# Optimization experiments

Measured on AMD Instinct MI355X. Metric: run time of the kernel, lower is better.

The kernel has to match this reference:

```python
import jax, jax.numpy as jnp
import numpy as np

DIM = 768
HEADS = 12
HEAD_DIM = DIM // HEADS
SCALE = HEAD_DIM ** -0.5


def setup_inputs() -> dict:
    key = jax.random.key(0)
    k_x, k_qkv, k_ow, k_ob = jax.random.split(key, 4)
    B, N = 8, 1024
    x = jax.random.normal(k_x, (B, N, DIM), dtype=jnp.float32)
    # nn.Linear weights: out = x @ W.T + b; store torch-layout [out, in]
    w_qkv = jax.random.normal(k_qkv, (3 * DIM, DIM), dtype=jnp.float32) * (DIM ** -0.5)
    w_out = jax.random.normal(k_ow, (DIM, DIM), dtype=jnp.float32) * (DIM ** -0.5)
    b_out = jax.random.normal(k_ob, (DIM,), dtype=jnp.float32) * 0.01
    return {"x": x, "w_qkv": w_qkv, "w_out": w_out, "b_out": b_out}


def reference(x, w_qkv, w_out, b_out):
    B, N, C = x.shape
    qkv = jnp.einsum('bnc,dc->bnd', x, w_qkv)            # [B, N, 3C]
    qkv = qkv.reshape(B, N, 3, HEADS, HEAD_DIM)
    qkv = jnp.transpose(qkv, (2, 0, 3, 1, 4))            # [3, B, H, N, Dh]
    q, k, v = qkv[0], qkv[1], qkv[2]
    attn = jnp.einsum('bhqd,bhkd->bhqk', q, k) * SCALE   # [B, H, N, N]
    attn = jax.nn.softmax(attn, axis=-1)
    o = jnp.einsum('bhqk,bhkd->bhqd', attn, v)           # [B, H, N, Dh]
    o = jnp.transpose(o, (0, 2, 1, 3)).reshape(B, N, C)
    return jnp.einsum('bnc,dc->bnd', o, w_out) + b_out
```

## Files before the change

### kernel.cpp

```cpp
#include <hip/hip_runtime.h>

#define B_ 8
#define N_ 1024
#define DIM_ 768
#define H_ 12
#define DH_ 64
#define M_ (B_ * N_)
#define NQKV_ (3 * DIM_)
#define SCL_ 0.18033688011112042f

typedef unsigned short u16;
typedef unsigned int u32;
typedef __attribute__((ext_vector_type(8))) unsigned short u16x8;
typedef __attribute__((ext_vector_type(4))) unsigned short u16x4;
typedef __attribute__((ext_vector_type(8))) short bf16x8;
typedef __attribute__((ext_vector_type(4))) float f32x4;

__device__ __forceinline__ u16 f2bf(float f) {
  u32 u = __builtin_bit_cast(u32, f);
  u += 0x7fffu + ((u >> 16) & 1u);
  return (u16)(u >> 16);
}
__device__ __forceinline__ float bf2f(u16 v) {
  u32 u = ((u32)v) << 16;
  return __builtin_bit_cast(float, u);
}
__device__ __forceinline__ u32 cvtpk_bf16(float lo, float hi) {
  u32 r;
  asm("v_cvt_pk_bf16_f32 %0, %1, %2" : "=v"(r) : "v"(lo), "v"(hi));
  return r;
}
__device__ __forceinline__ void async16(const void* g, void* l) {
  __builtin_amdgcn_global_load_lds(
      (const __attribute__((address_space(1))) unsigned int*)g,
      (__attribute__((address_space(3))) unsigned int*)l, 16, 0, 0);
}
#define WAIT4_BAR()                                     \
  asm volatile("s_waitcnt vmcnt(4)" ::: "memory");      \
  __builtin_amdgcn_s_barrier();                         \
  __builtin_amdgcn_sched_barrier(0)
#define WAIT0_BAR()                                     \
  asm volatile("s_waitcnt vmcnt(0)" ::: "memory");      \
  __builtin_amdgcn_s_barrier();                         \
  __builtin_amdgcn_sched_barrier(0)
#define RING_ADV(o) (o) = ((o) == 16384) ? 0 : (o) + 8192

__global__ __launch_bounds__(256) void cast_bf16_k(const float* __restrict__ in,
                                                   u16* __restrict__ out, int n4) {
  int i = blockIdx.x * 256 + threadIdx.x;
  if (i >= n4) return;
  float4 v = reinterpret_cast<const float4*>(in)[i];
  u16x4 o;
  o.x = f2bf(v.x); o.y = f2bf(v.y); o.z = f2bf(v.z); o.w = f2bf(v.w);
  reinterpret_cast<u16x4*>(out)[i] = o;
}

__device__ __forceinline__ void gemm_step(const char* lA, const char* lB,
                                          const int (&aoff)[4],
                                          const int (&boff)[4],
                                          f32x4 (&acc)[4][4]) {
  bf16x8 af[4], bfr[4];
#pragma unroll
  for (int m = 0; m < 4; ++m) af[m] = *(const bf16x8*)(lA + aoff[m]);
#pragma unroll
  for (int n = 0; n < 4; ++n) bfr[n] = *(const bf16x8*)(lB + boff[n]);
#pragma unroll
  for (int m = 0; m < 4; ++m)
#pragma unroll
    for (int n = 0; n < 4; ++n)
      acc[m][n] = __builtin_amdgcn_mfma_f32_16x16x32_bf16(af[m], bfr[n],
                                                          acc[m][n], 0, 0, 0);
}

template <bool OUT_BF16, bool BIAS, bool VSPLIT>
__global__ __launch_bounds__(256) void gemm_bt_k(
    const u16* __restrict__ A, const u16* __restrict__ Bm,
    void* __restrict__ Cv, const float* __restrict__ bias, int K, int ldc,
    u16* __restrict__ vT) {
  __shared__ u16 As[3][128 * 32];
  __shared__ u16 Bs[3][128 * 32];
  const int t = threadIdx.x;
  const int lane = t & 63;
  const int wid = t >> 6;
  const int id = blockIdx.x;
  const int xcd = id & 7, r = id >> 3;
  const int brow = ((xcd << 3) | (r & 7)) << 7;
  const int bcol = (r >> 3) << 7;
  const int wrow = (wid >> 1) << 6;
  const int wcol = (wid & 1) << 6;

  f32x4 acc[4][4];
#pragma unroll
  for (int m = 0; m < 4; ++m)
#pragma unroll
    for (int n = 0; n < 4; ++n) acc[m][n] = (f32x4){0.f, 0.f, 0.f, 0.f};

  const int loff0 = t << 4, loff1 = (t + 256) << 4;
  const int r0 = loff0 >> 6, r1 = loff1 >> 6;
  const int s0 = ((((loff0 >> 4) & 3) ^ (r0 & 3)) << 3);
  const int s1 = ((((loff1 >> 4) & 3) ^ (r1 & 3)) << 3);
  const u16* pA0 = A + (size_t)(brow + r0) * K + s0;
  const u16* pA1 = A + (size_t)(brow + r1) * K + s1;
  const u16* pB0 = Bm + (size_t)(bcol + r0) * K + s0;
  const u16* pB1 = Bm + (size_t)(bcol + r1) * K + s1;
  char* lA = (char*)As;
  char* lB = (char*)Bs;
  int sb = 0, cb = 0;

#define GSTAGE()                                  \
  do {                                            \
    async16(pA0, lA + sb + loff0);                \
    async16(pA1, lA + sb + loff1);                \
    async16(pB0, lB + sb + loff0);                \
    async16(pB1, lB + sb + loff1);                \
    pA0 += 32; pA1 += 32; pB0 += 32; pB1 += 32;   \
    RING_ADV(sb);                                 \
  } while (0)

  const int kb = (lane >> 4) << 4;
  int aoff[4], boff[4];
#pragma unroll
  for (int m = 0; m < 4; ++m) {
    int ra = wrow + (m << 4) + (lane & 15);
    aoff[m] = (ra << 6) + (kb ^ ((ra & 3) << 4));
    int rb = wcol + (m << 4) + (lane & 15);
    boff[m] = (rb << 6) + (kb ^ ((rb & 3) << 4));
  }

  const int nkt = K >> 5;
  GSTAGE();
  GSTAGE();
  for (int kt = 0; kt < nkt - 2; ++kt) {
    WAIT4_BAR();
    GSTAGE();
    gemm_step(lA + cb, lB + cb, aoff, boff, acc);
    RING_ADV(cb);
  }
  WAIT4_BAR();
  gemm_step(lA + cb, lB + cb, aoff, boff, acc);
  RING_ADV(cb);
  WAIT0_BAR();
  gemm_step(lA + cb, lB + cb, aoff, boff, acc);
#undef GSTAGE

  const int crow = brow + wrow + ((lane >> 4) << 2);
  const int ccol0 = bcol + wcol + (lane & 15);
  if (VSPLIT && bcol >= 2 * DIM_) {
#pragma unroll
    for (int n = 0; n < 4; ++n) {
      int colh = ccol0 + (n << 4) - 2 * DIM_;
      int h = colh >> 6, d = colh & 63;
#pragma unroll
      for (int m = 0; m < 4; ++m) {
        int row0 = crow + (m << 4);
        int bb = row0 >> 10, nn = row0 & 1023;
        int hbl = bb * H_ + h;
        uint2 pk;
        pk.x = (u32)f2bf(acc[m][n][0]) | ((u32)f2bf(acc[m][n][1]) << 16);
        pk.y = (u32)f2bf(acc[m][n][2]) | ((u32)f2bf(acc[m][n][3]) << 16);
        *(uint2*)(vT + (((size_t)(hbl * 64 + d)) << 10) + nn) = pk;
      }
    }
    return;
  }
#pragma unroll
  for (int m = 0; m < 4; ++m)
#pragma unroll
    for (int n = 0; n < 4; ++n) {
      int col = ccol0 + (n << 4);
      float bv = BIAS ? bias[col] : 0.f;
#pragma unroll
      for (int j = 0; j < 4; ++j) {
        int row = crow + (m << 4) + j;
        if (OUT_BF16)
          ((u16*)Cv)[(size_t)row * ldc + col] = f2bf(acc[m][n][j]);
        else
          ((float*)Cv)[(size_t)row * ldc + col] = acc[m][n][j] + bv;
      }
    }
}

__device__ __forceinline__ void attn_tile(const char* lk, const char* lv,
                                          char* lp, const bf16x8 (&qf)[2],
                                          f32x4 (&oacc)[4], float& mrow,
                                          float& lrow, const int rowB,
                                          const int xsw, const int x0,
                                          const int x1, const int g) {
  f32x4 s4[4];
#pragma unroll
  for (int n = 0; n < 4; ++n) s4[n] = (f32x4){0.f, 0.f, 0.f, 0.f};
  __builtin_amdgcn_s_setprio(1);
#pragma unroll
  for (int n = 0; n < 4; ++n) {
    bf16x8 kf0 = *(const bf16x8*)(lk + (n << 11) + rowB + x0);
    s4[n] = __builtin_amdgcn_mfma_f32_16x16x32_bf16(kf0, qf[0], s4[n], 0, 0, 0);
    bf16x8 kf1 = *(const bf16x8*)(lk + (n << 11) + rowB + x1);
    s4[n] = __builtin_amdgcn_mfma_f32_16x16x32_bf16(kf1, qf[1], s4[n], 0, 0, 0);
  }
  __builtin_amdgcn_s_setprio(0);

  float mx;
  {
    float a0 = fmaxf(fmaxf(s4[0][0], s4[0][1]), fmaxf(s4[0][2], s4[0][3]));
    float a1 = fmaxf(fmaxf(s4[1][0], s4[1][1]), fmaxf(s4[1][2], s4[1][3]));
    float a2 = fmaxf(fmaxf(s4[2][0], s4[2][1]), fmaxf(s4[2][2], s4[2][3]));
    float a3 = fmaxf(fmaxf(s4[3][0], s4[3][1]), fmaxf(s4[3][2], s4[3][3]));
    mx = fmaxf(fmaxf(a0, a1), fmaxf(a2, a3));
    mx = fmaxf(mx, __shfl_xor(mx, 16, 64));
    mx = fmaxf(mx, __shfl_xor(mx, 32, 64));
  }
  if (!__all(mx - mrow <= 8.f)) {
    float mn = fmaxf(mrow, mx);
    float al = __builtin_amdgcn_exp2f(mrow - mn);
    mrow = mn;
    lrow *= al;
    float alj[4];
#pragma unroll
    for (int j = 0; j < 4; ++j) alj[j] = __shfl(al, (g << 2) + j, 64);
#pragma unroll
    for (int d = 0; d < 4; ++d)
#pragma unroll
      for (int j = 0; j < 4; ++j) oacc[d][j] *= alj[j];
  }

  float p[4][4];
  float ps = 0.f;
#pragma unroll
  for (int n = 0; n < 4; ++n)
#pragma unroll
    for (int j = 0; j < 4; ++j) {
      p[n][j] = __builtin_amdgcn_exp2f(s4[n][j] - mrow);
      ps += p[n][j];
    }
  ps += __shfl_xor(ps, 16, 64);
  ps += __shfl_xor(ps, 32, 64);
  lrow += ps;

#pragma unroll
  for (int n = 0; n < 4; ++n) {
    uint2 pk;
    pk.x = cvtpk_bf16(p[n][0], p[n][1]);
    pk.y = cvtpk_bf16(p[n][2], p[n][3]);
    *(uint2*)(lp + rowB + (((n << 5) + (g << 3)) ^ xsw)) = pk;
  }

  bf16x8 pf0 = *(const bf16x8*)(lp + rowB + x0);
  bf16x8 pf1 = *(const bf16x8*)(lp + rowB + x1);
  __builtin_amdgcn_s_setprio(1);
#pragma unroll
  for (int dt = 0; dt < 4; ++dt) {
    bf16x8 vf0 = *(const bf16x8*)(lv + (dt << 11) + rowB + x0);
    oacc[dt] = __builtin_amdgcn_mfma_f32_16x16x32_bf16(pf0, vf0, oacc[dt], 0, 0, 0);
    bf16x8 vf1 = *(const bf16x8*)(lv + (dt << 11) + rowB + x1);
    oacc[dt] = __builtin_amdgcn_mfma_f32_16x16x32_bf16(pf1, vf1, oacc[dt], 0, 0, 0);
  }
  __builtin_amdgcn_s_setprio(0);
}

__global__ __launch_bounds__(256) void attn_k(const u16* __restrict__ qkv,
                                              const u16* __restrict__ vT,
                                              u16* __restrict__ ob) {
  __shared__ u16 Ks[3][64 * 64];
  __shared__ u16 Vt[3][64 * 64];
  __shared__ u16 Ps[4][16 * 64];
  const int t = threadIdx.x;
  const int lane = t & 63;
  const int w = t >> 6;
  const int g = lane >> 4;
  const int q15 = lane & 15;

  const int orig = blockIdx.x;
  const int sub = orig >> 3;
  const int hb = (orig & 7) * 12 + (sub >> 4);
  const int qt = sub & 15;
  const int b = hb / H_;
  const int h = hb - b * H_;
  const int rowbase = b * N_;
  const int qcol = h * DH_;
  const int kcol = DIM_ + qcol;

  bf16x8 qf[2];
  {
    const int qrow = rowbase + (qt << 6) + (w << 4) + q15;
    const u16* src = qkv + (size_t)qrow * NQKV_ + qcol + (g << 3);
#pragma unroll
    for (int ks = 0; ks < 2; ++ks) {
      u16x8 raw = *(const u16x8*)(src + ks * 32);
      bf16x8 o;
#pragma unroll
      for (int j = 0; j < 8; ++j) o[j] = (short)f2bf(bf2f(raw[j]) * SCL_);
      qf[ks] = o;
    }
  }

  float mrow = -1e30f, lrow = 0.f;
  f32x4 oacc[4];
#pragma unroll
  for (int d = 0; d < 4; ++d) oacc[d] = (f32x4){0.f, 0.f, 0.f, 0.f};

  const int sr = t >> 3;
  const int c8 = t & 7;
  const int loff0 = t << 4, loff1 = (t + 256) << 4;
  const u16* pk0 = qkv + (size_t)(rowbase + sr) * NQKV_ + kcol + ((c8 ^ (sr & 7)) << 3);
  const u16* pk1 = qkv + (size_t)(rowbase + sr + 32) * NQKV_ + kcol + ((c8 ^ (sr & 7)) << 3);
  const u16* pv0 = vT + (((size_t)(hb * 64 + sr)) << 10) + ((c8 ^ (sr & 7)) << 3);
  const u16* pv1 = vT + (((size_t)(hb * 64 + sr + 32)) << 10) + ((c8 ^ (sr & 7)) << 3);
  char* lk0 = (char*)Ks;
  char* lv0 = (char*)Vt;
  char* lp = (char*)Ps + (w << 11);
  int sb = 0, cb = 0;

#define ASTAGE()                                           \
  do {                                                     \
    async16(pk0, lk0 + sb + loff0);                        \
    async16(pk1, lk0 + sb + loff1);                        \
    async16(pv0, lv0 + sb + loff0);                        \
    async16(pv1, lv0 + sb + loff1);                        \
    pk0 += (size_t)64 * NQKV_; pk1 += (size_t)64 * NQKV_;  \
    pv0 += 64; pv1 += 64;                                  \
    RING_ADV(sb);                                          \
  } while (0)

  const int rowB = q15 << 7;
  const int xsw = (q15 & 7) << 4;
  const int x0 = (g << 4) ^ xsw;
  const int x1 = (64 + (g << 4)) ^ xsw;

  ASTAGE();
  ASTAGE();
  for (int kvt = 0; kvt < 14; ++kvt) {
    WAIT4_BAR();
    ASTAGE();
    attn_tile(lk0 + cb, lv0 + cb, lp, qf, oacc, mrow, lrow, rowB, xsw, x0, x1, g);
    RING_ADV(cb);
  }
  WAIT4_BAR();
  attn_tile(lk0 + cb, lv0 + cb, lp, qf, oacc, mrow, lrow, rowB, xsw, x0, x1, g);
  RING_ADV(cb);
  WAIT0_BAR();
  attn_tile(lk0 + cb, lv0 + cb, lp, qf, oacc, mrow, lrow, rowB, xsw, x0, x1, g);
#undef ASTAGE

  float rl = 1.f / lrow;
  float rlj[4];
#pragma unroll
  for (int j = 0; j < 4; ++j) rlj[j] = __shfl(rl, (g << 2) + j, 64);
  const int orow0 = rowbase + (qt << 6) + (w << 4) + (g << 2);
#pragma unroll
  for (int dt = 0; dt < 4; ++dt) {
    int col = qcol + (dt << 4) + q15;
#pragma unroll
    for (int j = 0; j < 4; ++j)
      ob[(size_t)(orow0 + j) * DIM_ + col] = f2bf(oacc[dt][j] * rlj[j]);
  }
}

extern "C" void kernel_launch(void* const* d_in, const int* in_sizes, int n_in,
                              void* d_out, int out_size, void* d_ws, size_t ws_size,
                              hipStream_t stream) {
  const float* x = (const float*)d_in[0];
  const float* w_qkv = (const float*)d_in[1];
  const float* w_out = (const float*)d_in[2];
  const float* b_out = (const float*)d_in[3];

  u16* xb = (u16*)d_ws;
  u16* wqkvb = xb + (size_t)M_ * DIM_;
  u16* woutb = wqkvb + (size_t)NQKV_ * DIM_;
  u16* qkvb = woutb + (size_t)DIM_ * DIM_;
  u16* obuf = qkvb + (size_t)M_ * NQKV_;
  u16* vT = obuf + (size_t)M_ * DIM_;

  {
    int n4 = M_ * DIM_ / 4;
    cast_bf16_k<<<(n4 + 255) / 256, 256, 0, stream>>>(x, xb, n4);
  }
  {
    int n4 = NQKV_ * DIM_ / 4;
    cast_bf16_k<<<(n4 + 255) / 256, 256, 0, stream>>>(w_qkv, wqkvb, n4);
  }
  {
    int n4 = DIM_ * DIM_ / 4;
    cast_bf16_k<<<(n4 + 255) / 256, 256, 0, stream>>>(w_out, woutb, n4);
  }

  gemm_bt_k<true, false, true><<<dim3((NQKV_ / 128) * (M_ / 128)), 256, 0, stream>>>(
      xb, wqkvb, (void*)qkvb, nullptr, DIM_, NQKV_, vT);

  attn_k<<<dim3(B_ * H_ * 16), 256, 0, stream>>>(qkvb, vT, obuf);

  gemm_bt_k<false, true, false><<<dim3((DIM_ / 128) * (M_ / 128)), 256, 0, stream>>>(
      obuf, woutb, d_out, b_out, DIM_, DIM_, nullptr);
}
```

Before: 214.1 us.

## Compute softmax row sums via MFMA and switch attention to double-buffered KV

The attention kernel now accumulates the softmax denominator with an extra MFMA that multiplies the bf16 P tile by a ones vector, replacing the per-tile VALU sum and cross-lane shuffles. The three-stage K/V ring buffer becomes a two-buffer ping-pong with compile-time buffer offsets and a full wait plus barrier after each tile. This is meant to cut VALU and shuffle work and address arithmetic and to reduce LDS use, which may help occupancy. In exchange, prefetch depth drops, so load latency may be hidden less well, and the row sum is now taken over bf16-rounded P values.

```diff
diff --git a/kernel.cpp b/kernel.cpp
--- a/kernel.cpp
+++ b/kernel.cpp
@@ -180,10 +180,11 @@
     }
 }
 
-__device__ __forceinline__ void attn_tile(const char* lk, const char* lv,
+template <int KOFF, int VOFF>
+__device__ __forceinline__ void attn_tile(const char* lk0, const char* lv0,
                                           char* lp, const bf16x8 (&qf)[2],
-                                          f32x4 (&oacc)[4], float& mrow,
-                                          float& lrow, const int rowB,
+                                          f32x4 (&oacc)[4], f32x4& lacc,
+                                          float& mrow, const int rowB,
                                           const int xsw, const int x0,
                                           const int x1, const int g) {
   f32x4 s4[4];
@@ -192,9 +193,9 @@
   __builtin_amdgcn_s_setprio(1);
 #pragma unroll
   for (int n = 0; n < 4; ++n) {
-    bf16x8 kf0 = *(const bf16x8*)(lk + (n << 11) + rowB + x0);
+    bf16x8 kf0 = *(const bf16x8*)(lk0 + KOFF + (n << 11) + rowB + x0);
     s4[n] = __builtin_amdgcn_mfma_f32_16x16x32_bf16(kf0, qf[0], s4[n], 0, 0, 0);
-    bf16x8 kf1 = *(const bf16x8*)(lk + (n << 11) + rowB + x1);
+    bf16x8 kf1 = *(const bf16x8*)(lk0 + KOFF + (n << 11) + rowB + x1);
     s4[n] = __builtin_amdgcn_mfma_f32_16x16x32_bf16(kf1, qf[1], s4[n], 0, 0, 0);
   }
   __builtin_amdgcn_s_setprio(0);
@@ -213,28 +214,23 @@
     float mn = fmaxf(mrow, mx);
     float al = __builtin_amdgcn_exp2f(mrow - mn);
     mrow = mn;
-    lrow *= al;
     float alj[4];
 #pragma unroll
     for (int j = 0; j < 4; ++j) alj[j] = __shfl(al, (g << 2) + j, 64);
 #pragma unroll
+    for (int j = 0; j < 4; ++j) lacc[j] *= alj[j];
+#pragma unroll
     for (int d = 0; d < 4; ++d)
 #pragma unroll
       for (int j = 0; j < 4; ++j) oacc[d][j] *= alj[j];
   }
 
   float p[4][4];
-  float ps = 0.f;
 #pragma unroll
   for (int n = 0; n < 4; ++n)
 #pragma unroll
-    for (int j = 0; j < 4; ++j) {
+    for (int j = 0; j < 4; ++j)
       p[n][j] = __builtin_amdgcn_exp2f(s4[n][j] - mrow);
-      ps += p[n][j];
-    }
-  ps += __shfl_xor(ps, 16, 64);
-  ps += __shfl_xor(ps, 32, 64);
-  lrow += ps;
 
 #pragma unroll
   for (int n = 0; n < 4; ++n) {
@@ -246,12 +242,16 @@
 
   bf16x8 pf0 = *(const bf16x8*)(lp + rowB + x0);
   bf16x8 pf1 = *(const bf16x8*)(lp + rowB + x1);
+  const bf16x8 ones = {0x3F80, 0x3F80, 0x3F80, 0x3F80,
+                       0x3F80, 0x3F80, 0x3F80, 0x3F80};
   __builtin_amdgcn_s_setprio(1);
+  lacc = __builtin_amdgcn_mfma_f32_16x16x32_bf16(pf0, ones, lacc, 0, 0, 0);
+  lacc = __builtin_amdgcn_mfma_f32_16x16x32_bf16(pf1, ones, lacc, 0, 0, 0);
 #pragma unroll
   for (int dt = 0; dt < 4; ++dt) {
-    bf16x8 vf0 = *(const bf16x8*)(lv + (dt << 11) + rowB + x0);
+    bf16x8 vf0 = *(const bf16x8*)(lv0 + VOFF + (dt << 11) + rowB + x0);
     oacc[dt] = __builtin_amdgcn_mfma_f32_16x16x32_bf16(pf0, vf0, oacc[dt], 0, 0, 0);
-    bf16x8 vf1 = *(const bf16x8*)(lv + (dt << 11) + rowB + x1);
+    bf16x8 vf1 = *(const bf16x8*)(lv0 + VOFF + (dt << 11) + rowB + x1);
     oacc[dt] = __builtin_amdgcn_mfma_f32_16x16x32_bf16(pf1, vf1, oacc[dt], 0, 0, 0);
   }
   __builtin_amdgcn_s_setprio(0);
@@ -260,8 +260,8 @@
 __global__ __launch_bounds__(256) void attn_k(const u16* __restrict__ qkv,
                                               const u16* __restrict__ vT,
                                               u16* __restrict__ ob) {
-  __shared__ u16 Ks[3][64 * 64];
-  __shared__ u16 Vt[3][64 * 64];
+  __shared__ u16 Ks[2][64 * 64];
+  __shared__ u16 Vt[2][64 * 64];
   __shared__ u16 Ps[4][16 * 64];
   const int t = threadIdx.x;
   const int lane = t & 63;
@@ -293,7 +293,8 @@
     }
   }
 
-  float mrow = -1e30f, lrow = 0.f;
+  float mrow = -1e30f;
+  f32x4 lacc = (f32x4){0.f, 0.f, 0.f, 0.f};
   f32x4 oacc[4];
 #pragma unroll
   for (int d = 0; d < 4; ++d) oacc[d] = (f32x4){0.f, 0.f, 0.f, 0.f};
@@ -308,17 +309,15 @@
   char* lk0 = (char*)Ks;
   char* lv0 = (char*)Vt;
   char* lp = (char*)Ps + (w << 11);
-  int sb = 0, cb = 0;
-
-#define ASTAGE()                                           \
+
+#define ASTAGE(BUFO)                                       \
   do {                                                     \
-    async16(pk0, lk0 + sb + loff0);                        \
-    async16(pk1, lk0 + sb + loff1);                        \
-    async16(pv0, lv0 + sb + loff0);                        \
-    async16(pv1, lv0 + sb + loff1);                        \
+    async16(pk0, lk0 + (BUFO) + loff0);                    \
+    async16(pk1, lk0 + (BUFO) + loff1);                    \
+    async16(pv0, lv0 + (BUFO) + loff0);                    \
+    async16(pv1, lv0 + (BUFO) + loff1);                    \
     pk0 += (size_t)64 * NQKV_; pk1 += (size_t)64 * NQKV_;  \
     pv0 += 64; pv1 += 64;                                  \
-    RING_ADV(sb);                                          \
   } while (0)
 
   const int rowB = q15 << 7;
@@ -326,32 +325,25 @@
   const int x0 = (g << 4) ^ xsw;
   const int x1 = (64 + (g << 4)) ^ xsw;
 
-  ASTAGE();
-  ASTAGE();
-  for (int kvt = 0; kvt < 14; ++kvt) {
-    WAIT4_BAR();
-    ASTAGE();
-    attn_tile(lk0 + cb, lv0 + cb, lp, qf, oacc, mrow, lrow, rowB, xsw, x0, x1, g);
-    RING_ADV(cb);
-  }
-  WAIT4_BAR();
-  attn_tile(lk0 + cb, lv0 + cb, lp, qf, oacc, mrow, lrow, rowB, xsw, x0, x1, g);
-  RING_ADV(cb);
+  ASTAGE(0);
   WAIT0_BAR();
-  attn_tile(lk0 + cb, lv0 + cb, lp, qf, oacc, mrow, lrow, rowB, xsw, x0, x1, g);
+  for (int kvt = 0; kvt < 16; kvt += 2) {
+    ASTAGE(8192);
+    attn_tile<0, 0>(lk0, lv0, lp, qf, oacc, lacc, mrow, rowB, xsw, x0, x1, g);
+    WAIT0_BAR();
+    if (kvt < 14) ASTAGE(0);
+    attn_tile<8192, 8192>(lk0, lv0, lp, qf, oacc, lacc, mrow, rowB, xsw, x0, x1, g);
+    WAIT0_BAR();
+  }
 #undef ASTAGE
 
-  float rl = 1.f / lrow;
-  float rlj[4];
-#pragma unroll
-  for (int j = 0; j < 4; ++j) rlj[j] = __shfl(rl, (g << 2) + j, 64);
   const int orow0 = rowbase + (qt << 6) + (w << 4) + (g << 2);
 #pragma unroll
   for (int dt = 0; dt < 4; ++dt) {
     int col = qcol + (dt << 4) + q15;
 #pragma unroll
     for (int j = 0; j < 4; ++j)
-      ob[(size_t)(orow0 + j) * DIM_ + col] = f2bf(oacc[dt][j] * rlj[j]);
+      ob[(size_t)(orow0 + j) * DIM_ + col] = f2bf(oacc[dt][j] / lacc[j]);
   }
 }
 
```

Result: faster. 197.1 us (-7.9%).
